# Kernel optimization log

Hardware: AMD Instinct MI355X
Metric: run time of the kernel (lower is better)

## Reference

```python
import jax, jax.numpy as jnp
import numpy as np

V, D, H = 50000, 256, 4
HD = H * D            # concat head dim (TransformerConv concat=True)
HH, O = 256, 256      # invariant_hidden_dim, invariant_out_dim
B, N, E, L, A = 16, 1000, 4000, 64, 128
PAD = 0
SCALE = 1.0 / float(np.sqrt(D))


def emb_lookup(table, idx):
    # nn.Embedding with padding_idx: forward is a plain gather; grad at pad row is zeroed.
    rows = table[idx]
    return jnp.where((idx == PAD)[..., None], jax.lax.stop_gradient(rows), rows)


def transformer_conv(x, edge_index, ea, Wq, bq, Wk, bk, Wv, bv, We, Wskip, bskip):
    # PyG TransformerConv, heads=H, concat=True, root_weight=True, beta=False, dropout=0 (eval)
    n = x.shape[0]
    src, dst = edge_index[0], edge_index[1]
    q = (x @ Wq + bq).reshape(n, H, D)
    e = (ea @ We).reshape(-1, H, D)          # lin_edge (bias=False)
    k = (x @ Wk + bk).reshape(n, H, D)[src] + e
    v = (x @ Wv + bv).reshape(n, H, D)[src] + e
    alpha = (q[dst] * k).sum(-1) * SCALE      # [E,H]
    amax = jax.ops.segment_max(alpha, dst, num_segments=n)
    ex = jnp.exp(alpha - amax[dst])
    denom = jax.ops.segment_sum(ex, dst, num_segments=n)
    w = ex / denom[dst]                       # per-target-node softmax over incoming edges
    agg = jax.ops.segment_sum(v * w[..., None], dst, num_segments=n)
    return agg.reshape(n, HD) + x @ Wskip + bskip  # lin_skip on root


def mixed_embed(tok, node, graph_repr, emb):
    fixed = emb_lookup(emb, tok)
    flex = jnp.take_along_axis(graph_repr, node[..., None], axis=1)
    flex = jnp.where((node == PAD)[..., None], jax.lax.stop_gradient(flex), flex)
    return fixed + flex


def gru_last(xs, W_ih, W_hh, b_ih, b_hh):
    # torch nn.GRU, batch_first, 1 layer; only last hidden state is used
    gx = jnp.einsum('blh,gh->blg', xs, W_ih) + b_ih  # [B,L,3O]

    def step(h, g):
        gh = h @ W_hh.T + b_hh
        xr, xz, xn = jnp.split(g, 3, axis=-1)
        hr, hz, hn = jnp.split(gh, 3, axis=-1)
        r = jax.nn.sigmoid(xr + hr)
        z = jax.nn.sigmoid(xz + hz)
        c = jnp.tanh(xn + r * hn)
        return (1.0 - z) * c + z * h, None

    h0 = jnp.zeros((xs.shape[0], W_hh.shape[1]), xs.dtype)
    h_last, _ = jax.lax.scan(step, h0, jnp.swapaxes(gx, 0, 1))
    return h_last


def setup_inputs() -> dict:
    key = jax.random.key(0)
    ks = jax.random.split(key, 40)
    f = lambda i, shape, s=0.05: jax.random.normal(ks[i], shape, jnp.float32) * s
    ri = lambda i, shape, hi: jax.random.randint(ks[i], shape, 0, hi)
    return {
        'node_tokens': ri(0, (B, N), V),
        'edge_tokens': ri(1, (B, E), V),
        'edge_index': ri(2, (B, 2, E), N),
        'inv_token': ri(3, (B, L), V),
        'inv_node': ri(4, (B, L), N),
        'aa_token': ri(5, (B, A), V),
        'aa_node': ri(6, (B, A), N),
        'action_mask': jnp.ones((B, A), jnp.float32),
        'emb': f(7, (V, D), 0.02),
        'Wq': f(8, (D, HD)), 'bq': f(9, (HD,)),
        'Wk': f(10, (D, HD)), 'bk': f(11, (HD,)),
        'Wv': f(12, (D, HD)), 'bv': f(13, (HD,)),
        'We': f(14, (D, HD)),
        'Wskip': f(15, (D, HD)), 'bskip': f(16, (HD,)),
        'W1': f(17, (HD, D)), 'b1': f(18, (D,)),
        'Wp': f(19, (D, HH)), 'bp': f(20, (HH,)),
        'W_ih': f(21, (3 * O, HH)), 'W_hh': f(22, (3 * O, O)),
        'b_ih': f(23, (3 * O,)), 'b_hh': f(24, (3 * O,)),
        'Wab': f(25, (D, 1)), 'bab': f(26, (1,)),
        'Wap': f(27, (D, O)), 'bap': f(28, (O,)),
    }


def reference(node_tokens, edge_tokens, edge_index, inv_token, inv_node, aa_token, aa_node,
              action_mask, emb, Wq, bq, Wk, bk, Wv, bv, We, Wskip, bskip, W1, b1,
              Wp, bp, W_ih, W_hh, b_ih, b_hh, Wab, bab, Wap, bap):
    x = emb_lookup(emb, node_tokens)    # [B,N,D]
    ea = emb_lookup(emb, edge_tokens)   # [B,E,D]
    conv = jax.vmap(lambda xx, ei, ee: transformer_conv(
        xx, ei, ee, Wq, bq, Wk, bk, Wv, bv, We, Wskip, bskip))
    h = jax.nn.relu(conv(x, edge_index, ea))            # [B,N,HD]
    graph_repr = jax.nn.relu(h @ W1 + b1)               # [B,N,D]
    inv_h = jax.nn.relu(mixed_embed(inv_token, inv_node, graph_repr, emb) @ Wp + bp)
    inv = gru_last(inv_h, W_ih, W_hh, b_ih, b_hh)       # [B,O]
    aa_emb = mixed_embed(aa_token, aa_node, graph_repr, emb)  # [B,A,D]
    scores = jnp.einsum('bao,bo->ba', aa_emb @ Wap + bap, inv) + (aa_emb @ Wab + bab)[..., 0]
    inf_mask = jnp.maximum(jnp.log(action_mask), jnp.float32(np.finfo(np.float32).min))
    return scores + inf_mask
```

## Files before the change

### kernel.cpp

```cpp
#include <hip/hip_runtime.h>
#include <hip/hip_bf16.h>
#include <float.h>
#include <math.h>

typedef __hip_bfloat16 bf16;

#define B_ 16
#define N_ 1000
#define E_ 4000
#define L_ 64
#define A_ 128
#define D_ 256
#define H_ 4
#define HD_ 1024
#define SCALE_ 0.0625f

typedef __attribute__((ext_vector_type(8))) short short8;
typedef __attribute__((ext_vector_type(4))) float f32x4;

union U4S8 { uint4 u; short8 s; };

__device__ __forceinline__ unsigned short f2bf(float f) {
    bf16 h = __float2bfloat16(f);
    return *reinterpret_cast<unsigned short*>(&h);
}
__device__ __forceinline__ unsigned pack2(float a, float b) {
    return (unsigned)f2bf(a) | ((unsigned)f2bf(b) << 16);
}
__device__ __forceinline__ unsigned short rne1(float a) {
    unsigned ua = __float_as_uint(a);
    ua += 0x7fff + ((ua >> 16) & 1);
    return (unsigned short)(ua >> 16);
}
__device__ __forceinline__ float bflo(unsigned u) { return __uint_as_float(u << 16); }
__device__ __forceinline__ float bfhi(unsigned u) { return __uint_as_float(u & 0xffff0000u); }

#define LOG2E 1.4426950408889634f
__device__ __forceinline__ float fsigm(float x) {
    return __builtin_amdgcn_rcpf(1.f + __builtin_amdgcn_exp2f(-LOG2E * x));
}
__device__ __forceinline__ float ftanh(float x) {
    return 1.f - 2.f * __builtin_amdgcn_rcpf(1.f + __builtin_amdgcn_exp2f(2.f * LOG2E * x));
}

typedef const __attribute__((address_space(1))) unsigned int* gas_t;
typedef __attribute__((address_space(3))) unsigned int* las_t;
__device__ __forceinline__ void gld16(const void* g, void* l) {
    __builtin_amdgcn_global_load_lds((gas_t)g, (las_t)l, 16, 0, 0);
}

__global__ void convemb_kernel(const float* __restrict__ src, bf16* __restrict__ dst, long n4)
{
    long i = (long)blockIdx.x * 256 + threadIdx.x;
    if (i >= n4) return;
    float4 v = *(const float4*)(src + i * 4);
    *(uint2*)(dst + i * 4) = make_uint2(pack2(v.x, v.y), pack2(v.z, v.w));
}

__global__ void pack_all_kernel(const float* __restrict__ Wq, const float* __restrict__ Wk,
                                const float* __restrict__ Wv, const float* __restrict__ Wskip,
                                const float* __restrict__ We, const float* __restrict__ W1,
                                const float* __restrict__ Wp, const float* __restrict__ W_ih,
                                const float* __restrict__ Wap, const float* __restrict__ W_hh,
                                const float* __restrict__ bq, const float* __restrict__ bk,
                                const float* __restrict__ bv, const float* __restrict__ bskip,
                                unsigned* __restrict__ qkvsP, unsigned* __restrict__ WeP,
                                unsigned* __restrict__ W1P, unsigned* __restrict__ WpP,
                                unsigned* __restrict__ WihP, unsigned* __restrict__ WeTP,
                                short8* __restrict__ WhhP, float* __restrict__ bias4096)
{
    int i = blockIdx.x * 256 + threadIdx.x;
    if (i < 524288) {
        int k2 = i >> 12, n = i & 4095;
        const float* s = (n < 1024) ? Wq : (n < 2048) ? Wk : (n < 3072) ? Wv : Wskip;
        int col = n & 1023;
        qkvsP[i] = pack2(s[(long)(2 * k2) * 1024 + col], s[(long)(2 * k2 + 1) * 1024 + col]);
        return;
    }
    i -= 524288;
    if (i < 131072) {
        int k2 = i >> 10, n = i & 1023;
        WeP[i] = pack2(We[(long)(2 * k2) * 1024 + n], We[(long)(2 * k2 + 1) * 1024 + n]);
        return;
    }
    i -= 131072;
    if (i < 131072) {
        int k2 = i >> 8, n = i & 255;
        W1P[i] = pack2(W1[(long)(2 * k2) * 256 + n], W1[(long)(2 * k2 + 1) * 256 + n]);
        return;
    }
    i -= 131072;
    if (i < 32768) {
        int k2 = i >> 8, n = i & 255;
        WpP[i] = pack2(Wp[(long)(2 * k2) * 256 + n], Wp[(long)(2 * k2 + 1) * 256 + n]);
        return;
    }
    i -= 32768;
    if (i < 98304) {
        int k2 = i / 768, n = i % 768;
        WihP[i] = pack2(W_ih[(long)n * 256 + 2 * k2], W_ih[(long)n * 256 + 2 * k2 + 1]);
        return;
    }
    i -= 98304;
    if (i < 131072) {
        int k2 = i >> 10, n = i & 1023;
        int d = n & 255, hb = n & ~255;
        WeTP[i] = pack2(We[(long)d * 1024 + hb + 2 * k2],
                        We[(long)d * 1024 + hb + 2 * k2 + 1]);
        return;
    }
    i -= 131072;
    if (i < 24576) {
        int lane = i & 63, tk = (i >> 6) & 7, tile = i >> 9;
        int n = tile * 16 + (lane & 15);
        const float* wp = W_hh + (long)n * 256 + tk * 32 + (lane >> 4) * 8;
        float4 w0 = *(const float4*)wp;
        float4 w1 = *(const float4*)(wp + 4);
        U4S8 u;
        u.u = make_uint4(pack2(w0.x, w0.y), pack2(w0.z, w0.w),
                         pack2(w1.x, w1.y), pack2(w1.z, w1.w));
        WhhP[i] = u.s;
        return;
    }
    i -= 24576;
    if (i < 4096) {
        int q = i >> 10, c = i & 1023;
        bias4096[i] = ((q == 0) ? bq : (q == 1) ? bk : (q == 2) ? bv : bskip)[c];
    }
}
#define PACK_ALL_TOT (524288 + 131072 + 131072 + 32768 + 98304 + 131072 + 24576 + 4096)

#define TM 128
#define TN 128
#define TK 32
#define BSTR 132

template <typename CT>
__global__ __launch_bounds__(256)
void pgemm_kernel(const bf16* __restrict__ A, const int* __restrict__ arows,
                  const unsigned* __restrict__ Bp, const float* __restrict__ bias,
                  CT* __restrict__ C, int M, int K, int Nc, int relu_out,
                  long astride, int aoff, int colbase, int hslice, int addC, int outT)
{
    __shared__ short    As[TM * TK];
    __shared__ unsigned Bs[(TK / 2) * BSTR];

    const int tid  = threadIdx.x;
    const int lane = tid & 63;
    const int wave = tid >> 6;
    const int wm = wave >> 1, wn = wave & 1;
    const int quad = lane >> 4, c16 = lane & 15;
    const long row0 = (long)blockIdx.y * TM;
    const int  col0 = colbase + blockIdx.x * TN;
    const int  aoff2 = aoff + (hslice ? (col0 & ~255) : 0);

    const int r0 = wave * 32 + (lane >> 2);
    const int cseg = (lane & 3) * 8;
    long gr0 = row0 + r0;      if (gr0 > M - 1) gr0 = M - 1;
    long gr1 = row0 + r0 + 16; if (gr1 > M - 1) gr1 = M - 1;
    long ar0 = arows ? (long)arows[gr0] : gr0;
    long ar1 = arows ? (long)arows[gr1] : gr1;
    const short* Ag0 = (const short*)A + ar0 * astride + aoff2 + cseg;
    const short* Ag1 = (const short*)A + ar1 * astride + aoff2 + cseg;
    short* Ld0 = &As[wave * 1024];
    short* Ld1 = &As[wave * 1024 + 512];

    const int sn2 = tid & 63;
    const int skk = wave * 4;

    f32x4 acc[4][4];
    #pragma unroll
    for (int i = 0; i < 4; ++i)
        #pragma unroll
        for (int j = 0; j < 4; ++j)
            acc[i][j] = (f32x4){0.f, 0.f, 0.f, 0.f};

    for (int k0 = 0; k0 < K; k0 += TK) {
        gld16(Ag0 + k0, Ld0);
        gld16(Ag1 + k0, Ld1);
        #pragma unroll
        for (int i = 0; i < 4; ++i) {
            int kk2 = skk + i;
            *(uint2*)&Bs[kk2 * BSTR + sn2 * 2] =
                *(const uint2*)&Bp[(long)(k0 / 2 + kk2) * Nc + col0 + sn2 * 2];
        }
        __syncthreads();

        short8 af[4];
        U4S8   bfr[4];
        #pragma unroll
        for (int mi = 0; mi < 4; ++mi) {
            int m = wm * 64 + mi * 16 + c16;
            af[mi] = *(const short8*)&As[m * 32 + quad * 8];
        }
        #pragma unroll
        for (int ni = 0; ni < 4; ++ni) {
            int n = wn * 64 + ni * 16 + c16;
            uint4 u;
            u.x = Bs[(quad * 4 + 0) * BSTR + n];
            u.y = Bs[(quad * 4 + 1) * BSTR + n];
            u.z = Bs[(quad * 4 + 2) * BSTR + n];
            u.w = Bs[(quad * 4 + 3) * BSTR + n];
            bfr[ni].u = u;
        }
        #pragma unroll
        for (int mi = 0; mi < 4; ++mi)
            #pragma unroll
            for (int ni = 0; ni < 4; ++ni)
                acc[mi][ni] = __builtin_amdgcn_mfma_f32_16x16x32_bf16(
                    af[mi], bfr[ni].s, acc[mi][ni], 0, 0, 0);
        __syncthreads();
    }

    #pragma unroll
    for (int ni = 0; ni < 4; ++ni) {
        int col = col0 + wn * 64 + ni * 16 + c16;
        float bv = bias ? bias[col] : 0.f;
        #pragma unroll
        for (int mi = 0; mi < 4; ++mi) {
            long row = row0 + wm * 64 + mi * 16 + quad * 4;
            #pragma unroll
            for (int r = 0; r < 4; ++r) {
                if (row + r >= M) continue;
                float v = acc[mi][ni][r] + bv;
                if (addC) v += (float)C[(row + r) * Nc + col];
                if (relu_out) v = fmaxf(v, 0.f);
                if (outT) {
                    long rr = row + r;
                    int t = (int)(rr & 63), b = (int)(rr >> 6);
                    C[((long)t * Nc + col) * 16 + b] = (CT)v;
                } else {
                    C[(row + r) * Nc + col] = (CT)v;
                }
            }
        }
    }
}

__global__ __launch_bounds__(1024)
void csr_kernel(const int* __restrict__ edge_index, int b0,
                int* __restrict__ row_start, int* __restrict__ cntg,
                int* __restrict__ elist)
{
    int bl = blockIdx.x;
    int tid = threadIdx.x;
    __shared__ int scnt[1024];
    __shared__ int sscan[1024];

    scnt[tid] = 0;
    __syncthreads();

    const int* dstp = edge_index + (long)(b0 + bl) * 2 * E_ + E_;
    #pragma unroll
    for (int e = tid; e < E_; e += 1024)
        atomicAdd(&scnt[dstp[e]], 1);
    __syncthreads();

    int v = scnt[tid];
    sscan[tid] = v;
    __syncthreads();
    for (int off = 1; off < 1024; off <<= 1) {
        int t = (tid >= off) ? sscan[tid - off] : 0;
        __syncthreads();
        sscan[tid] += t;
        __syncthreads();
    }
    int excl = sscan[tid] - v;
    if (tid < N_) {
        row_start[bl * N_ + tid] = excl;
        cntg[bl * N_ + tid] = v;
    }
    __syncthreads();
    scnt[tid] = excl;
    __syncthreads();

    int* el = elist + (long)bl * E_;
    #pragma unroll
    for (int e = tid; e < E_; e += 1024) {
        int pos = atomicAdd(&scnt[dstp[e]], 1);
        el[pos] = e;
    }
}

__device__ __forceinline__ float d2(unsigned a, unsigned b)
{
    return bflo(a) * bflo(b) + bfhi(a) * bfhi(b);
}

__global__ void attn_kernel(const bf16* __restrict__ qkvs, const bf16* __restrict__ qWb,
                            const bf16* __restrict__ embh,
                            const int* __restrict__ edge_tokens, const int* __restrict__ edge_index,
                            const int* __restrict__ row_start, const int* __restrict__ cnt,
                            const int* __restrict__ elist, int b0,
                            bf16* __restrict__ aggb, bf16* __restrict__ xsumb)
{
    int base = blockIdx.x;
    int bl = base / N_;
    int tid = threadIdx.x;
    int l = tid & 63;
    int j0 = tid * 4;
    int jx = l * 4;

    uint2 qq = *(const uint2*)(qkvs + (long)base * 4096 + j0);
    uint2 ww = *(const uint2*)(qWb + (long)base * 1024 + j0);

    int start = row_start[base];
    int deg = cnt[base];
    const int* el = elist + (long)bl * E_;
    const int* srcp = edge_index + (long)(b0 + bl) * 2 * E_;
    const int* tokp = edge_tokens + (long)(b0 + bl) * E_;

    float denom = 0.f;
    float v0 = 0.f, v1 = 0.f, v2 = 0.f, v3 = 0.f;
    float x0 = 0.f, x1 = 0.f, x2 = 0.f, x3 = 0.f;

    int t = 0;
    while (t + 1 < deg) {
        int ea = el[start + t], eb2 = el[start + t + 1];
        int sa = srcp[ea], sb = srcp[eb2];
        int ta = tokp[ea], tb = tokp[eb2];
        const bf16* ra = qkvs + (long)(bl * N_ + sa) * 4096;
        const bf16* rb = qkvs + (long)(bl * N_ + sb) * 4096;
        uint2 ka = *(const uint2*)(ra + 1024 + j0);
        uint2 kb = *(const uint2*)(rb + 1024 + j0);
        uint2 va = *(const uint2*)(ra + 2048 + j0);
        uint2 vb = *(const uint2*)(rb + 2048 + j0);
        uint2 xa = *(const uint2*)(embh + (long)ta * 256 + jx);
        uint2 xb = *(const uint2*)(embh + (long)tb * 256 + jx);

        float s1 = d2(qq.x, ka.x) + d2(qq.y, ka.y) + d2(ww.x, xa.x) + d2(ww.y, xa.y);
        float s2 = d2(qq.x, kb.x) + d2(qq.y, kb.y) + d2(ww.x, xb.x) + d2(ww.y, xb.y);
        s1 += __shfl_xor(s1, 32);  s2 += __shfl_xor(s2, 32);
        s1 += __shfl_xor(s1, 16);  s2 += __shfl_xor(s2, 16);
        s1 += __shfl_xor(s1, 8);   s2 += __shfl_xor(s2, 8);
        s1 += __shfl_xor(s1, 4);   s2 += __shfl_xor(s2, 4);
        s1 += __shfl_xor(s1, 2);   s2 += __shfl_xor(s2, 2);
        s1 += __shfl_xor(s1, 1);   s2 += __shfl_xor(s2, 1);
        float exa = __builtin_amdgcn_exp2f(s1 * (SCALE_ * LOG2E));
        float exb = __builtin_amdgcn_exp2f(s2 * (SCALE_ * LOG2E));

        denom += exa + exb;
        v0 += exa * bflo(va.x) + exb * bflo(vb.x);
        v1 += exa * bfhi(va.x) + exb * bfhi(vb.x);
        v2 += exa * bflo(va.y) + exb * bflo(vb.y);
        v3 += exa * bfhi(va.y) + exb * bfhi(vb.y);
        x0 += exa * bflo(xa.x) + exb * bflo(xb.x);
        x1 += exa * bfhi(xa.x) + exb * bfhi(xb.x);
        x2 += exa * bflo(xa.y) + exb * bflo(xb.y);
        x3 += exa * bfhi(xa.y) + exb * bfhi(xb.y);
        t += 2;
    }
    if (t < deg) {
        int ea = el[start + t];
        int sa = srcp[ea], ta = tokp[ea];
        const bf16* ra = qkvs + (long)(bl * N_ + sa) * 4096;
        uint2 ka = *(const uint2*)(ra + 1024 + j0);
        uint2 va = *(const uint2*)(ra + 2048 + j0);
        uint2 xa = *(const uint2*)(embh + (long)ta * 256 + jx);
        float s1 = d2(qq.x, ka.x) + d2(qq.y, ka.y) + d2(ww.x, xa.x) + d2(ww.y, xa.y);
        s1 += __shfl_xor(s1, 32);
        s1 += __shfl_xor(s1, 16);
        s1 += __shfl_xor(s1, 8);
        s1 += __shfl_xor(s1, 4);
        s1 += __shfl_xor(s1, 2);
        s1 += __shfl_xor(s1, 1);
        float exa = __builtin_amdgcn_exp2f(s1 * (SCALE_ * LOG2E));
        denom += exa;
        v0 += exa * bflo(va.x); v1 += exa * bfhi(va.x);
        v2 += exa * bflo(va.y); v3 += exa * bfhi(va.y);
        x0 += exa * bflo(xa.x); x1 += exa * bfhi(xa.x);
        x2 += exa * bflo(xa.y); x3 += exa * bfhi(xa.y);
    }

    float invd = (deg > 0) ? 1.f / denom : 0.f;
    uint2 sk = *(const uint2*)(qkvs + (long)base * 4096 + 3072 + j0);
    unsigned o0 = pack2(bflo(sk.x) + v0 * invd, bfhi(sk.x) + v1 * invd);
    unsigned o1 = pack2(bflo(sk.y) + v2 * invd, bfhi(sk.y) + v3 * invd);
    *(uint2*)(aggb + (long)base * HD_ + j0) = make_uint2(o0, o1);
    *(uint2*)(xsumb + (long)base * HD_ + j0) =
        make_uint2(pack2(x0 * invd, x1 * invd), pack2(x2 * invd, x3 * invd));
}

__global__ void mixed2_kernel(const bf16* __restrict__ embh,
                              const int* __restrict__ inv_token, const int* __restrict__ inv_node,
                              const int* __restrict__ aa_token, const int* __restrict__ aa_node,
                              const bf16* __restrict__ graph_repr,
                              bf16* __restrict__ mixed_inv, bf16* __restrict__ aa_emb)
{
    int r = blockIdx.x;
    int d = threadIdx.x;
    if (r < B_ * L_) {
        int b = r / L_;
        float v = (float)embh[(long)inv_token[r] * D_ + d] +
                  (float)graph_repr[((long)b * N_ + inv_node[r]) * D_ + d];
        mixed_inv[(long)r * D_ + d] = __float2bfloat16(v);
    } else {
        int r2 = r - B_ * L_;
        int b = r2 / A_;
        float v = (float)embh[(long)aa_token[r2] * D_ + d] +
                  (float)graph_repr[((long)b * N_ + aa_node[r2]) * D_ + d];
        aa_emb[(long)r2 * D_ + d] = __float2bfloat16(v);
    }
}

__global__ __launch_bounds__(1024)
void gru_kernel(const bf16* __restrict__ gxT, const short8* __restrict__ WhhP,
                const float* __restrict__ b_hh, float* __restrict__ inv_out)
{
    __shared__ short hB[2][16 * 264];

    const int tid = threadIdx.x;
    const int lane = tid & 63;
    const int wave = tid >> 6;
    const int quad = lane >> 4, c16 = lane & 15;
    const int n0 = wave * 16 + c16;
    const int bb = blockIdx.x * 4 + quad;

    for (int i = tid; i < 2 * 16 * 264; i += 1024) ((short*)hB)[i] = 0;

    short8 wfr[8], wfz[8], wfn[8];
    #pragma unroll
    for (int tk = 0; tk < 8; ++tk) {
        wfr[tk] = WhhP[((0 * 16 + wave) * 8 + tk) * 64 + lane];
        wfz[tk] = WhhP[((1 * 16 + wave) * 8 + tk) * 64 + lane];
        wfn[tk] = WhhP[((2 * 16 + wave) * 8 + tk) * 64 + lane];
    }
    float bhr = b_hh[0 * 256 + n0];
    float bhz = b_hh[1 * 256 + n0];
    float bhn = b_hh[2 * 256 + n0];

    float myh = 0.f;

    const unsigned short* g_r = (const unsigned short*)gxT + (long)n0 * 16 + bb;
    const unsigned short* g_z = g_r + 256 * 16;
    const unsigned short* g_n = g_r + 512 * 16;

    unsigned short pr = g_r[0], pz = g_z[0], pn = g_n[0];

    __syncthreads();

    int p = 0;
    for (int t = 0; t < L_; ++t) {
        float xr = __uint_as_float((unsigned)pr << 16);
        float xz = __uint_as_float((unsigned)pz << 16);
        float xn = __uint_as_float((unsigned)pn << 16);
        long noff = (long)((t + 1 < L_) ? t + 1 : t) * 12288;
        pr = g_r[noff]; pz = g_z[noff]; pn = g_n[noff];

        f32x4 ar = (f32x4){bhr, bhr, bhr, bhr};
        f32x4 az = (f32x4){bhz, bhz, bhz, bhz};
        f32x4 an = (f32x4){bhn, bhn, bhn, bhn};
        const short* hp = &hB[p][0];
        #pragma unroll
        for (int tk = 0; tk < 8; ++tk) {
            short8 a = *(const short8*)&hp[c16 * 264 + tk * 32 + quad * 8];
            ar = __builtin_amdgcn_mfma_f32_16x16x32_bf16(a, wfr[tk], ar, 0, 0, 0);
            az = __builtin_amdgcn_mfma_f32_16x16x32_bf16(a, wfz[tk], az, 0, 0, 0);
            an = __builtin_amdgcn_mfma_f32_16x16x32_bf16(a, wfn[tk], an, 0, 0, 0);
        }

        float rr = fsigm(xr + ar[0]);
        float zz = fsigm(xz + az[0]);
        float cc = ftanh(xn + rr * an[0]);
        myh = (1.f - zz) * cc + zz * myh;
        hB[p ^ 1][(quad * 4) * 264 + n0] = (short)rne1(myh);
        p ^= 1;
        __syncthreads();
    }

    inv_out[(long)bb * 256 + n0] = myh;
}

__global__ void uprep_kernel(const float* __restrict__ Wap, const float* __restrict__ Wab,
                             const float* __restrict__ bap, const float* __restrict__ bab,
                             const float* __restrict__ inv, float* __restrict__ u,
                             float* __restrict__ s0)
{
    int b = blockIdx.x, d = threadIdx.x;
    __shared__ float iv[256];
    iv[d] = inv[(long)b * 256 + d];
    __syncthreads();
    float s = Wab[d];
    const float* wr = Wap + (long)d * 256;
    #pragma unroll 8
    for (int o = 0; o < 256; ++o) s += wr[o] * iv[o];
    u[(long)b * 256 + d] = s;
    if (d == 0) {
        float t = bab[0];
        for (int o = 0; o < 256; ++o) t += bap[o] * iv[o];
        s0[b] = t;
    }
}

__global__ void score_kernel(const bf16* __restrict__ aa_emb, const float* __restrict__ u,
                             const float* __restrict__ s0, const float* __restrict__ mask,
                             float* __restrict__ out)
{
    int r = blockIdx.x * 4 + (threadIdx.x >> 6);
    int l = threadIdx.x & 63;
    int b = r / A_;
    float s = 0.f;
    for (int d = l; d < D_; d += 64)
        s += (float)aa_emb[(long)r * D_ + d] * u[(long)b * D_ + d];
    #pragma unroll
    for (int off = 32; off; off >>= 1) s += __shfl_down(s, off);
    if (l == 0) {
        float lm = logf(mask[r]);
        const float MN = -3.4028234663852886e38f;
        if (!(lm >= MN)) lm = MN;
        out[r] = s + s0[b] + lm;
    }
}

static inline size_t align256(size_t x) { return (x + 255) & ~(size_t)255; }

template <typename CT>
static void launch_pgemm(const bf16* A, const int* arows, const unsigned* Bp,
                         const float* bias, CT* C, int M, int K, int Nc, int relu,
                         long astride, int aoff, int colbase, int hslice, int addC,
                         int outT, int ncols, hipStream_t s)
{
    dim3 grid(ncols / TN, (M + TM - 1) / TM);
    pgemm_kernel<CT><<<grid, 256, 0, s>>>(A, arows, Bp, bias, C, M, K, Nc, relu,
                                          astride, aoff, colbase, hslice, addC, outT);
}

extern "C" void kernel_launch(void* const* d_in, const int* in_sizes, int n_in,
                              void* d_out, int out_size, void* d_ws, size_t ws_size,
                              hipStream_t stream)
{
    const int* node_tokens = (const int*)d_in[0];
    const int* edge_tokens = (const int*)d_in[1];
    const int* edge_index  = (const int*)d_in[2];
    const int* inv_token   = (const int*)d_in[3];
    const int* inv_node    = (const int*)d_in[4];
    const int* aa_token    = (const int*)d_in[5];
    const int* aa_node     = (const int*)d_in[6];
    const float* action_mask = (const float*)d_in[7];
    const float* emb   = (const float*)d_in[8];
    const float* Wq    = (const float*)d_in[9];
    const float* bq    = (const float*)d_in[10];
    const float* Wk    = (const float*)d_in[11];
    const float* bk    = (const float*)d_in[12];
    const float* Wv    = (const float*)d_in[13];
    const float* bv    = (const float*)d_in[14];
    const float* We    = (const float*)d_in[15];
    const float* Wskip = (const float*)d_in[16];
    const float* bskip = (const float*)d_in[17];
    const float* W1    = (const float*)d_in[18];
    const float* b1    = (const float*)d_in[19];
    const float* Wp    = (const float*)d_in[20];
    const float* bp    = (const float*)d_in[21];
    const float* W_ih  = (const float*)d_in[22];
    const float* W_hh  = (const float*)d_in[23];
    const float* b_ih  = (const float*)d_in[24];
    const float* b_hh  = (const float*)d_in[25];
    const float* Wab   = (const float*)d_in[26];
    const float* bab   = (const float*)d_in[27];
    const float* Wap   = (const float*)d_in[28];
    const float* bap   = (const float*)d_in[29];
    (void)in_sizes; (void)n_in; (void)out_size;

    char* base = (char*)d_ws;
    size_t off = 0;
    auto alloc = [&](size_t bytes) -> char* {
        char* p = base + off;
        off = align256(off + bytes);
        return p;
    };

    const long VD = 50000L * 256;
    bf16*  embh       = (bf16*)alloc(VD * 2);
    bf16*  graph_repr = (bf16*)alloc((size_t)B_ * N_ * D_ * 2);
    bf16*  mixed_inv  = (bf16*)alloc((size_t)B_ * L_ * D_ * 2);
    bf16*  inv_h      = (bf16*)alloc((size_t)B_ * L_ * D_ * 2);
    bf16*  gxT        = (bf16*)alloc((size_t)B_ * L_ * 768 * 2);
    float* inv_out    = (float*)alloc((size_t)B_ * 256 * 4);
    bf16*  aa_emb     = (bf16*)alloc((size_t)B_ * A_ * D_ * 2);
    float* ubuf       = (float*)alloc((size_t)B_ * 256 * 4);
    float* s0buf      = (float*)alloc((size_t)B_ * 4);
    unsigned* qkvsP   = (unsigned*)alloc((size_t)128 * 4096 * 4);
    unsigned* WeP     = (unsigned*)alloc((size_t)128 * 1024 * 4);
    unsigned* W1P     = (unsigned*)alloc((size_t)512 * 256 * 4);
    unsigned* WpP     = (unsigned*)alloc((size_t)128 * 256 * 4);
    unsigned* WihP    = (unsigned*)alloc((size_t)128 * 768 * 4);
    unsigned* WeTP    = (unsigned*)alloc((size_t)128 * 1024 * 4);
    short8* WhhP      = (short8*)alloc((size_t)24576 * 16);
    float* bias4096   = (float*)alloc(4096 * 4);
    size_t persist = off;

    int c = 16;
    while (c > 1) {
        size_t cN = (size_t)c * N_, cEs = (size_t)c * E_;
        size_t chunk = align256(cN * 4096 * 2)
                     + align256(cN * HD_ * 2)
                     + align256(cN * HD_ * 2)
                     + align256(cN * HD_ * 2)
                     + 2 * align256(cN * 4)
                     + align256(cEs * 4);
        if (persist + chunk <= ws_size) break;
        c >>= 1;
    }
    int cN = c * N_, cE = c * E_;

    bf16*  qkvs  = (bf16*)alloc((size_t)cN * 4096 * 2);
    bf16*  qWb   = (bf16*)alloc((size_t)cN * HD_ * 2);
    bf16*  aggb  = (bf16*)alloc((size_t)cN * HD_ * 2);
    bf16*  xsumb = (bf16*)alloc((size_t)cN * HD_ * 2);
    int*   cnt   = (int*)alloc((size_t)cN * 4);
    int*   rstart= (int*)alloc((size_t)cN * 4);
    int*   elist = (int*)alloc((size_t)cE * 4);

    convemb_kernel<<<(int)((VD / 4 + 255) / 256), 256, 0, stream>>>(emb, embh, VD / 4);
    pack_all_kernel<<<(PACK_ALL_TOT + 255) / 256, 256, 0, stream>>>(
        Wq, Wk, Wv, Wskip, We, W1, Wp, W_ih, Wap, W_hh, bq, bk, bv, bskip,
        qkvsP, WeP, W1P, WpP, WihP, WeTP, WhhP, bias4096);

    for (int b0 = 0; b0 < B_; b0 += c) {
        csr_kernel<<<c, 1024, 0, stream>>>(edge_index, b0, rstart, cnt, elist);
        launch_pgemm<bf16>(embh, node_tokens + (long)b0 * N_, qkvsP, bias4096, qkvs,
                           cN, D_, 4096, 0, 256, 0, 0, 0, 0, 0, 4096, stream);
        launch_pgemm<bf16>(qkvs, nullptr, WeTP, nullptr, qWb,
                           cN, 256, 1024, 0, 4096, 0, 0, 1, 0, 0, 1024, stream);
        attn_kernel<<<cN, 256, 0, stream>>>(qkvs, qWb, embh, edge_tokens, edge_index,
                                            rstart, cnt, elist, b0, aggb, xsumb);
        launch_pgemm<bf16>(xsumb, nullptr, WeP, nullptr, aggb,
                           cN, 256, 1024, 1, 1024, 0, 0, 1, 1, 0, 1024, stream);
        launch_pgemm<bf16>(aggb, nullptr, W1P, b1,
                           graph_repr + (long)b0 * N_ * D_,
                           cN, HD_, D_, 1, 1024, 0, 0, 0, 0, 0, 256, stream);
    }

    mixed2_kernel<<<B_ * L_ + B_ * A_, 256, 0, stream>>>(embh, inv_token, inv_node,
                                                         aa_token, aa_node, graph_repr,
                                                         mixed_inv, aa_emb);
    launch_pgemm<bf16>(mixed_inv, nullptr, WpP, bp, inv_h,
                       B_ * L_, D_, 256, 1, 256, 0, 0, 0, 0, 0, 256, stream);
    launch_pgemm<bf16>(inv_h, nullptr, WihP, b_ih, gxT,
                       B_ * L_, 256, 768, 0, 256, 0, 0, 0, 0, 1, 768, stream);
    gru_kernel<<<4, 1024, 0, stream>>>(gxT, WhhP, b_hh, inv_out);

    uprep_kernel<<<B_, 256, 0, stream>>>(Wap, Wab, bap, bab, inv_out, ubuf, s0buf);
    score_kernel<<<(B_ * A_) / 4, 256, 0, stream>>>(aa_emb, ubuf, s0buf,
                                                    action_mask, (float*)d_out);
}
```

Measured before the change: 787.5 us.

## Fold per-head q·We product into QKV projection weights, drop separate qWb GEMM

```diff
diff --git a/kernel.cpp b/kernel.cpp
--- a/kernel.cpp
+++ b/kernel.cpp
@@ -14,6 +14,7 @@
 #define H_ 4
 #define HD_ 1024
 #define SCALE_ 0.0625f
+#define QS 5120
 
 typedef __attribute__((ext_vector_type(8))) short short8;
 typedef __attribute__((ext_vector_type(4))) float f32x4;
@@ -61,20 +62,21 @@
                                 const float* __restrict__ Wv, const float* __restrict__ Wskip,
                                 const float* __restrict__ We, const float* __restrict__ W1,
                                 const float* __restrict__ Wp, const float* __restrict__ W_ih,
-                                const float* __restrict__ Wap, const float* __restrict__ W_hh,
+                                const float* __restrict__ W_hh,
                                 const float* __restrict__ bq, const float* __restrict__ bk,
                                 const float* __restrict__ bv, const float* __restrict__ bskip,
                                 unsigned* __restrict__ qkvsP, unsigned* __restrict__ WeP,
                                 unsigned* __restrict__ W1P, unsigned* __restrict__ WpP,
-                                unsigned* __restrict__ WihP, unsigned* __restrict__ WeTP,
-                                short8* __restrict__ WhhP, float* __restrict__ bias4096)
+                                unsigned* __restrict__ WihP,
+                                short8* __restrict__ WhhP, float* __restrict__ bias5120)
 {
     int i = blockIdx.x * 256 + threadIdx.x;
     if (i < 524288) {
         int k2 = i >> 12, n = i & 4095;
         const float* s = (n < 1024) ? Wq : (n < 2048) ? Wk : (n < 3072) ? Wv : Wskip;
         int col = n & 1023;
-        qkvsP[i] = pack2(s[(long)(2 * k2) * 1024 + col], s[(long)(2 * k2 + 1) * 1024 + col]);
+        qkvsP[(long)k2 * QS + n] =
+            pack2(s[(long)(2 * k2) * 1024 + col], s[(long)(2 * k2 + 1) * 1024 + col]);
         return;
     }
     i -= 524288;
@@ -102,14 +104,6 @@
         return;
     }
     i -= 98304;
-    if (i < 131072) {
-        int k2 = i >> 10, n = i & 1023;
-        int d = n & 255, hb = n & ~255;
-        WeTP[i] = pack2(We[(long)d * 1024 + hb + 2 * k2],
-                        We[(long)d * 1024 + hb + 2 * k2 + 1]);
-        return;
-    }
-    i -= 131072;
     if (i < 24576) {
         int lane = i & 63, tk = (i >> 6) & 7, tile = i >> 9;
         int n = tile * 16 + (lane & 15);
@@ -125,10 +119,40 @@
     i -= 24576;
     if (i < 4096) {
         int q = i >> 10, c = i & 1023;
-        bias4096[i] = ((q == 0) ? bq : (q == 1) ? bk : (q == 2) ? bv : bskip)[c];
-    }
-}
-#define PACK_ALL_TOT (524288 + 131072 + 131072 + 32768 + 98304 + 131072 + 24576 + 4096)
+        bias5120[i] = ((q == 0) ? bq : (q == 1) ? bk : (q == 2) ? bv : bskip)[c];
+    }
+}
+#define PACK_ALL_TOT (524288 + 131072 + 131072 + 32768 + 98304 + 24576 + 4096)
+
+__global__ __launch_bounds__(256)
+void wqe_kernel(const float* __restrict__ Wq, const float* __restrict__ We,
+                const float* __restrict__ bq,
+                unsigned* __restrict__ qkvsP, float* __restrict__ bias5120)
+{
+    int k2 = blockIdx.x >> 2;
+    int h  = blockIdx.x & 3;
+    int d  = threadIdx.x;
+    int hb = h * 256;
+    __shared__ float w0[256], w1[256];
+    w0[d] = Wq[(long)(2 * k2) * 1024 + hb + d];
+    w1[d] = Wq[(long)(2 * k2 + 1) * 1024 + hb + d];
+    __syncthreads();
+    const float* wer = We + (long)d * 1024 + hb;
+    float s0 = 0.f, s1 = 0.f;
+    #pragma unroll 8
+    for (int j = 0; j < 256; ++j) {
+        float we = wer[j];
+        s0 += w0[j] * we;
+        s1 += w1[j] * we;
+    }
+    qkvsP[(long)k2 * QS + 4096 + hb + d] = pack2(s0, s1);
+    if (k2 == 0) {
+        float t = 0.f;
+        const float* bqh = bq + hb;
+        for (int j = 0; j < 256; ++j) t += bqh[j] * wer[j];
+        bias5120[4096 + hb + d] = t;
+    }
+}
 
 #define TM 128
 #define TN 128
@@ -228,7 +252,7 @@
                 if (outT) {
                     long rr = row + r;
                     int t = (int)(rr & 63), b = (int)(rr >> 6);
-                    C[((long)t * Nc + col) * 16 + b] = (CT)v;
+                    C[(((long)(b >> 2) * 64 + t) * Nc + col) * 4 + (b & 3)] = (CT)v;
                 } else {
                     C[(row + r) * Nc + col] = (CT)v;
                 }
@@ -287,7 +311,7 @@
     return bflo(a) * bflo(b) + bfhi(a) * bfhi(b);
 }
 
-__global__ void attn_kernel(const bf16* __restrict__ qkvs, const bf16* __restrict__ qWb,
+__global__ void attn_kernel(const bf16* __restrict__ qkvs,
                             const bf16* __restrict__ embh,
                             const int* __restrict__ edge_tokens, const int* __restrict__ edge_index,
                             const int* __restrict__ row_start, const int* __restrict__ cnt,
@@ -301,8 +325,8 @@
     int j0 = tid * 4;
     int jx = l * 4;
 
-    uint2 qq = *(const uint2*)(qkvs + (long)base * 4096 + j0);
-    uint2 ww = *(const uint2*)(qWb + (long)base * 1024 + j0);
+    uint2 qq = *(const uint2*)(qkvs + (long)base * QS + j0);
+    uint2 ww = *(const uint2*)(qkvs + (long)base * QS + 4096 + j0);
 
     int start = row_start[base];
     int deg = cnt[base];
@@ -319,8 +343,8 @@
         int ea = el[start + t], eb2 = el[start + t + 1];
         int sa = srcp[ea], sb = srcp[eb2];
         int ta = tokp[ea], tb = tokp[eb2];
-        const bf16* ra = qkvs + (long)(bl * N_ + sa) * 4096;
-        const bf16* rb = qkvs + (long)(bl * N_ + sb) * 4096;
+        const bf16* ra = qkvs + (long)(bl * N_ + sa) * QS;
+        const bf16* rb = qkvs + (long)(bl * N_ + sb) * QS;
         uint2 ka = *(const uint2*)(ra + 1024 + j0);
         uint2 kb = *(const uint2*)(rb + 1024 + j0);
         uint2 va = *(const uint2*)(ra + 2048 + j0);
@@ -353,7 +377,7 @@
     if (t < deg) {
         int ea = el[start + t];
         int sa = srcp[ea], ta = tokp[ea];
-        const bf16* ra = qkvs + (long)(bl * N_ + sa) * 4096;
+        const bf16* ra = qkvs + (long)(bl * N_ + sa) * QS;
         uint2 ka = *(const uint2*)(ra + 1024 + j0);
         uint2 va = *(const uint2*)(ra + 2048 + j0);
         uint2 xa = *(const uint2*)(embh + (long)ta * 256 + jx);
@@ -373,7 +397,7 @@
     }
 
     float invd = (deg > 0) ? 1.f / denom : 0.f;
-    uint2 sk = *(const uint2*)(qkvs + (long)base * 4096 + 3072 + j0);
+    uint2 sk = *(const uint2*)(qkvs + (long)base * QS + 3072 + j0);
     unsigned o0 = pack2(bflo(sk.x) + v0 * invd, bfhi(sk.x) + v1 * invd);
     unsigned o1 = pack2(bflo(sk.y) + v2 * invd, bfhi(sk.y) + v3 * invd);
     *(uint2*)(aggb + (long)base * HD_ + j0) = make_uint2(o0, o1);
@@ -431,9 +455,10 @@
 
     float myh = 0.f;
 
-    const unsigned short* g_r = (const unsigned short*)gxT + (long)n0 * 16 + bb;
-    const unsigned short* g_z = g_r + 256 * 16;
-    const unsigned short* g_n = g_r + 512 * 16;
+    const unsigned short* g_r = (const unsigned short*)gxT +
+        ((long)blockIdx.x * 64 * 768 + n0) * 4 + quad;
+    const unsigned short* g_z = g_r + 256 * 4;
+    const unsigned short* g_n = g_r + 512 * 4;
 
     unsigned short pr = g_r[0], pz = g_z[0], pn = g_n[0];
 
@@ -444,7 +469,7 @@
         float xr = __uint_as_float((unsigned)pr << 16);
         float xz = __uint_as_float((unsigned)pz << 16);
         float xn = __uint_as_float((unsigned)pn << 16);
-        long noff = (long)((t + 1 < L_) ? t + 1 : t) * 12288;
+        long noff = (long)((t + 1 < L_) ? t + 1 : t) * 3072;
         pr = g_r[noff]; pz = g_z[noff]; pn = g_n[noff];
 
         f32x4 ar = (f32x4){bhr, bhr, bhr, bhr};
@@ -579,21 +604,19 @@
     bf16*  aa_emb     = (bf16*)alloc((size_t)B_ * A_ * D_ * 2);
     float* ubuf       = (float*)alloc((size_t)B_ * 256 * 4);
     float* s0buf      = (float*)alloc((size_t)B_ * 4);
-    unsigned* qkvsP   = (unsigned*)alloc((size_t)128 * 4096 * 4);
+    unsigned* qkvsP   = (unsigned*)alloc((size_t)128 * QS * 4);
     unsigned* WeP     = (unsigned*)alloc((size_t)128 * 1024 * 4);
     unsigned* W1P     = (unsigned*)alloc((size_t)512 * 256 * 4);
     unsigned* WpP     = (unsigned*)alloc((size_t)128 * 256 * 4);
     unsigned* WihP    = (unsigned*)alloc((size_t)128 * 768 * 4);
-    unsigned* WeTP    = (unsigned*)alloc((size_t)128 * 1024 * 4);
     short8* WhhP      = (short8*)alloc((size_t)24576 * 16);
-    float* bias4096   = (float*)alloc(4096 * 4);
+    float* bias5120   = (float*)alloc(QS * 4);
     size_t persist = off;
 
     int c = 16;
     while (c > 1) {
         size_t cN = (size_t)c * N_, cEs = (size_t)c * E_;
-        size_t chunk = align256(cN * 4096 * 2)
-                     + align256(cN * HD_ * 2)
+        size_t chunk = align256(cN * QS * 2)
                      + align256(cN * HD_ * 2)
                      + align256(cN * HD_ * 2)
                      + 2 * align256(cN * 4)
@@ -603,8 +626,7 @@
     }
     int cN = c * N_, cE = c * E_;
 
-    bf16*  qkvs  = (bf16*)alloc((size_t)cN * 4096 * 2);
-    bf16*  qWb   = (bf16*)alloc((size_t)cN * HD_ * 2);
+    bf16*  qkvs  = (bf16*)alloc((size_t)cN * QS * 2);
     bf16*  aggb  = (bf16*)alloc((size_t)cN * HD_ * 2);
     bf16*  xsumb = (bf16*)alloc((size_t)cN * HD_ * 2);
     int*   cnt   = (int*)alloc((size_t)cN * 4);
@@ -613,16 +635,15 @@
 
     convemb_kernel<<<(int)((VD / 4 + 255) / 256), 256, 0, stream>>>(emb, embh, VD / 4);
     pack_all_kernel<<<(PACK_ALL_TOT + 255) / 256, 256, 0, stream>>>(
-        Wq, Wk, Wv, Wskip, We, W1, Wp, W_ih, Wap, W_hh, bq, bk, bv, bskip,
-        qkvsP, WeP, W1P, WpP, WihP, WeTP, WhhP, bias4096);
+        Wq, Wk, Wv, Wskip, We, W1, Wp, W_ih, W_hh, bq, bk, bv, bskip,
+        qkvsP, WeP, W1P, WpP, WihP, WhhP, bias5120);
+    wqe_kernel<<<512, 256, 0, stream>>>(Wq, We, bq, qkvsP, bias5120);
 
     for (int b0 = 0; b0 < B_; b0 += c) {
         csr_kernel<<<c, 1024, 0, stream>>>(edge_index, b0, rstart, cnt, elist);
-        launch_pgemm<bf16>(embh, node_tokens + (long)b0 * N_, qkvsP, bias4096, qkvs,
-                           cN, D_, 4096, 0, 256, 0, 0, 0, 0, 0, 4096, stream);
-        launch_pgemm<bf16>(qkvs, nullptr, WeTP, nullptr, qWb,
-                           cN, 256, 1024, 0, 4096, 0, 0, 1, 0, 0, 1024, stream);
-        attn_kernel<<<cN, 256, 0, stream>>>(qkvs, qWb, embh, edge_tokens, edge_index,
+        launch_pgemm<bf16>(embh, node_tokens + (long)b0 * N_, qkvsP, bias5120, qkvs,
+                           cN, D_, QS, 0, 256, 0, 0, 0, 0, 0, QS, stream);
+        attn_kernel<<<cN, 256, 0, stream>>>(qkvs, embh, edge_tokens, edge_index,
                                             rstart, cnt, elist, b0, aggb, xsumb);
         launch_pgemm<bf16>(xsumb, nullptr, WeP, nullptr, aggb,
                            cN, 256, 1024, 1, 1024, 0, 0, 1, 1, 0, 1024, stream);
```

Measured after the change: 755.8 us, median of 3. -4.0%, faster.
